# Performance work log

Measured on AMD Instinct MI355X. Metric: run time of the kernel, lower is better.

## Reference

```python
import jax, jax.numpy as jnp
import numpy as np
import math

B, L, C = 2, 4096, 256
H = 4            # n_head
K = 4            # Chebyshev kernel size
GROUPS = 32      # GroupNorm groups
EPS = 1e-5


def group_norm(x, gamma, beta):
    # x: [B, L, C]; stats per (batch, group) over (L, C//G), as torch GroupNorm
    # applied to x.permute(0, 2, 1) -> [B, C, L].
    b, l, c = x.shape
    xg = x.reshape(b, l, GROUPS, c // GROUPS)
    mean = xg.mean(axis=(1, 3), keepdims=True)
    var = xg.var(axis=(1, 3), keepdims=True)
    xg = (xg - mean) * jax.lax.rsqrt(var + EPS)
    return xg.reshape(b, l, c) * gamma + beta


def cheb_conv(lap, x, w):
    # Chebyshev graph conv: x [B, L, Fin], lap [L, L], w [K, Fin, Fout]
    xt = [x]
    if w.shape[0] > 1:
        xt.append(jnp.einsum('uv,bvc->buc', lap, x))
    for _ in range(2, w.shape[0]):
        xt.append(2.0 * jnp.einsum('uv,bvc->buc', lap, xt[-1]) - xt[-2])
    xs = jnp.stack(xt, axis=0)                       # [K, B, L, Fin]
    return jnp.einsum('kblc,kcf->blf', xs, w)        # [B, L, Fout]


def setup_inputs() -> dict:
    key = jax.random.key(0)
    ks = jax.random.split(key, 4)
    x = jax.random.normal(ks[0], (B, L, C), dtype=jnp.float32)
    # symmetric, spectrally well-behaved stand-in Laplacian
    a = jax.random.normal(ks[1], (L, L), dtype=jnp.float32) / jnp.sqrt(jnp.float32(L))
    lap = 0.5 * (a + a.T)
    gamma = jnp.ones((C,), dtype=jnp.float32)
    beta = jnp.zeros((C,), dtype=jnp.float32)
    w_qkv = jax.random.normal(ks[2], (K, C, 3 * C), dtype=jnp.float32) * (1.0 / math.sqrt(C * K))
    w_out = jax.random.normal(ks[3], (K, C, C), dtype=jnp.float32) * (1.0 / math.sqrt(C * K))
    return {"x": x, "lap": lap, "gamma": gamma, "beta": beta,
            "w_qkv": w_qkv, "w_out": w_out}


def reference(x, lap, gamma, beta, w_qkv, w_out):
    b, l, c = x.shape
    hd = c // H
    norm = group_norm(x, gamma, beta)
    qkv = cheb_conv(lap, norm, w_qkv).reshape(b, l, H, 3 * hd)
    q, k, v = jnp.split(qkv, 3, axis=3)              # each [B, L, H, hd]
    attn = jnp.einsum('blnc,bmnc->blmn', q, k) / math.sqrt(c)  # [B, L, M, H]
    # faithful to torch: view(B, L, H, -1) re-splits contiguous (M, H) as (H, M)
    attn = jax.nn.softmax(attn.reshape(b, l, H, -1), axis=-1)
    attn = attn.reshape(b, l, l, H)
    out = jnp.einsum('blmn,bmnc->blnc', attn, v).reshape(b, l, c)
    out = cheb_conv(lap, out, w_out)
    return out + x
```

## Files before the change

### kernel.cpp

```cpp
#include <hip/hip_runtime.h>
#include <hip/hip_bf16.h>
#include <stdint.h>

#define L 4096
#define C 256
#define NH 4
#define F3 768
#define KC 1024

typedef __attribute__((ext_vector_type(4))) float f32x4;
typedef __attribute__((ext_vector_type(8))) short short8;
typedef unsigned short u16;

__device__ __forceinline__ u16 f2bf(float f) {
  union { float f; unsigned u; } v; v.f = f;
  unsigned r = v.u + 0x7FFFu + ((v.u >> 16) & 1u);
  return (u16)(r >> 16);
}
__device__ __forceinline__ float bf2f(u16 b) {
  union { unsigned u; float f; } v; v.u = ((unsigned)b) << 16;
  return v.f;
}
__device__ __forceinline__ u16 f2bf_rne(float f) {
  __hip_bfloat16 h = __float2bfloat16(f);
  return *(u16*)&h;
}

__device__ __forceinline__ void glds16(const u16* g, u16* lds_base_uniform) {
  __builtin_amdgcn_global_load_lds(
      (const __attribute__((address_space(1))) void*)g,
      (__attribute__((address_space(3))) void*)lds_base_uniform, 16, 0, 0);
}


__global__ __launch_bounds__(256) void tobf16_kernel(const float* __restrict__ src, u16* __restrict__ dst, long n) {
  long i = ((long)blockIdx.x * 256 + threadIdx.x) * 8;
  if (i >= n) return;
  float4 a = *(const float4*)(src + i);
  float4 c = *(const float4*)(src + i + 4);
  u16 o[8] = {f2bf(a.x),f2bf(a.y),f2bf(a.z),f2bf(a.w),f2bf(c.x),f2bf(c.y),f2bf(c.z),f2bf(c.w)};
  *(int4*)(dst + i) = *(int4*)o;
}

__global__ __launch_bounds__(256) void transpose_w_kernel(const float* __restrict__ src, u16* __restrict__ dst, int F) {
  int idx = blockIdx.x * 256 + threadIdx.x;
  if (idx >= F * KC) return;
  int f = idx / KC, kc = idx - f * KC;
  dst[idx] = f2bf(src[(long)kc * F + f]);
}

__global__ __launch_bounds__(256) void gn_stats(const float* __restrict__ x, float* __restrict__ st) {
  const int b = blockIdx.x >> 5, g = blockIdx.x & 31, ch = blockIdx.y;
  const int tid = threadIdx.x;
  const float* xb = x + (long)b * L * C + g * 8;
  float s = 0.f, sq = 0.f;
  for (int l = ch * 512 + tid; l < ch * 512 + 512; l += 256) {
    const float4* p = (const float4*)(xb + (long)l * C);
    float4 a = p[0], c = p[1];
    s  += a.x + a.y + a.z + a.w + c.x + c.y + c.z + c.w;
    sq += a.x*a.x + a.y*a.y + a.z*a.z + a.w*a.w + c.x*c.x + c.y*c.y + c.z*c.z + c.w*c.w;
  }
  __shared__ float rs[256], rq[256];
  rs[tid] = s; rq[tid] = sq;
  __syncthreads();
  for (int o = 128; o > 0; o >>= 1) {
    if (tid < o) { rs[tid] += rs[tid + o]; rq[tid] += rq[tid + o]; }
    __syncthreads();
  }
  if (tid == 0) {
    st[(blockIdx.x * 8 + ch) * 2 + 0] = rs[0];
    st[(blockIdx.x * 8 + ch) * 2 + 1] = rq[0];
  }
}

__global__ __launch_bounds__(256) void gn_apply(const float* __restrict__ x, const float* __restrict__ gamma,
                                                const float* __restrict__ beta, const float* __restrict__ st,
                                                u16* __restrict__ normT, u16* __restrict__ xt_nt) {
  const int b = blockIdx.x >> 5, g = blockIdx.x & 31, ch = blockIdx.y;
  const int tid = threadIdx.x;
  float s = 0.f, sq = 0.f;
#pragma unroll
  for (int j = 0; j < 8; ++j) {
    s  += st[(blockIdx.x * 8 + j) * 2 + 0];
    sq += st[(blockIdx.x * 8 + j) * 2 + 1];
  }
  const float mean = s * (1.f / 32768.f);
  const float var  = sq * (1.f / 32768.f) - mean * mean;
  const float rsig = rsqrtf(var + 1e-5f);
  float gm[8], bt[8];
#pragma unroll
  for (int j = 0; j < 8; ++j) { gm[j] = gamma[g*8+j] * rsig; bt[j] = beta[g*8+j]; }
  const float* xb = x + (long)b * L * C + g * 8;
  for (int l = ch * 512 + tid; l < ch * 512 + 512; l += 256) {
    const float4* p = (const float4*)(xb + (long)l * C);
    float4 a = p[0], c = p[1];
    float v[8] = {a.x,a.y,a.z,a.w,c.x,c.y,c.z,c.w};
    u16 o8[8];
#pragma unroll
    for (int j = 0; j < 8; ++j) o8[j] = f2bf((v[j] - mean) * gm[j] + bt[j]);
    *(int4*)(xt_nt + ((long)b * L + l) * KC + g * 8) = *(int4*)o8;
#pragma unroll
    for (int j = 0; j < 8; ++j) normT[(long)(b * C + g * 8 + j) * L + l] = o8[j];
  }
}

#define BM 128
#define BN 128
#define BK 64

template<int OUT_BF16, int QSCALE, int SPLITK>
__global__ __launch_bounds__(256) void gemm_bt(const u16* __restrict__ A, const u16* __restrict__ BT,
                                               void* __restrict__ Cv, int M, int N, int Kc, int Ktot) {
  __shared__ u16 Al[BM * BK];
  __shared__ u16 Bl[BN * BK];
  const int tid = threadIdx.x;
  const int lane = tid & 63;
  const int wid = tid >> 6;
  const int wr = (wid >> 1) * 64;
  const int wc = (wid & 1) * 64;
  const long bm = (long)blockIdx.x * BM;
  const long bn = (long)blockIdx.y * BN;
  const int k_beg = SPLITK ? blockIdx.z * Kc : 0;
  const int k_end = k_beg + Kc;
  const int jrow = lane & 15, jk = lane >> 4;
  const int lr8 = lane >> 3, lsl = lane & 7;
  f32x4 acc[4][4] = {};

  for (int k0 = k_beg; k0 < k_end; k0 += BK) {
#pragma unroll
    for (int j = 0; j < 4; ++j) {
      int chunk = wid * 4 + j;
      int r = chunk * 8 + lr8;
      glds16(A + (bm + r) * (long)Ktot + k0 + ((lsl ^ (r & 7)) * 8), Al + chunk * 512);
    }
#pragma unroll
    for (int j = 0; j < 4; ++j) {
      int chunk = wid * 4 + j;
      int r = chunk * 8 + lr8;
      glds16(BT + (bn + r) * (long)Ktot + k0 + ((lsl ^ (r & 7)) * 8), Bl + chunk * 512);
    }
    __syncthreads();
    short8 af[4][2], bfr[4][2];
#pragma unroll
    for (int rt = 0; rt < 4; ++rt)
#pragma unroll
      for (int kc = 0; kc < 2; ++kc) {
        int r = wr + rt * 16 + jrow;
        int sl = kc * 4 + jk;
        af[rt][kc] = *(short8*)(Al + r * 64 + ((sl ^ (r & 7)) * 8));
      }
#pragma unroll
    for (int ct = 0; ct < 4; ++ct)
#pragma unroll
      for (int kc = 0; kc < 2; ++kc) {
        int r = wc + ct * 16 + jrow;
        int sl = kc * 4 + jk;
        bfr[ct][kc] = *(short8*)(Bl + r * 64 + ((sl ^ (r & 7)) * 8));
      }
#pragma unroll
    for (int kc = 0; kc < 2; ++kc)
#pragma unroll
      for (int rt = 0; rt < 4; ++rt)
#pragma unroll
        for (int ct = 0; ct < 4; ++ct)
          acc[rt][ct] = __builtin_amdgcn_mfma_f32_16x16x32_bf16(af[rt][kc], bfr[ct][kc], acc[rt][ct], 0, 0, 0);
    __syncthreads();
  }
  float* outf = SPLITK ? ((float*)Cv + (long)blockIdx.z * M * N) : (float*)Cv;
#pragma unroll
  for (int rt = 0; rt < 4; ++rt)
#pragma unroll
    for (int ct = 0; ct < 4; ++ct)
#pragma unroll
      for (int r = 0; r < 4; ++r) {
        long row = bm + wr + rt * 16 + 4 * jk + r;
        long col = bn + wc + ct * 16 + jrow;
        float v = acc[rt][ct][r];
        if (QSCALE) { if ((int)(col % 192) < 64) v *= 0.0625f; }
        if (OUT_BF16) ((u16*)Cv)[row * N + col] = f2bf(v);
        else outf[row * N + col] = v;
      }
}

__global__ __launch_bounds__(256) void cheb_combine(const float* __restrict__ Yp, const u16* __restrict__ prevT,
                                                    u16* __restrict__ outT, u16* __restrict__ xt_nt,
                                                    int kslot, float coef) {
  __shared__ u16 t[64][65];
  const int r0 = blockIdx.x * 64, c0 = blockIdx.y * 64;
  const int tid = threadIdx.x;
  const long pl = 512L * L;
#pragma unroll
  for (int s = 0; s < 16; ++s) {
    int idx = s * 256 + tid;
    int r = idx >> 6, c = idx & 63;
    long off = (long)(r0 + r) * L + c0 + c;
    float v = coef * (Yp[off] + Yp[pl + off] + Yp[2 * pl + off] + Yp[3 * pl + off]);
    if (prevT) v -= bf2f(prevT[off]);
    u16 u = f2bf(v);
    outT[off] = u;
    t[r][c] = u;
  }
  __syncthreads();
  const int b = r0 >> 8, ch0 = r0 & 255;
#pragma unroll
  for (int s = 0; s < 16; ++s) {
    int idx = s * 256 + tid;
    int lr = idx >> 6, cc = idx & 63;
    xt_nt[((long)b * L + c0 + lr) * KC + kslot * C + ch0 + cc] = t[cc][lr];
  }
}

__global__ __launch_bounds__(256) void out_combine(const float* __restrict__ Yp, const float* __restrict__ x,
                                                   float* __restrict__ out) {
  const long pl = 2097152L;
  long i = ((long)blockIdx.x * 256 + threadIdx.x) * 4;
  float4 a = *(const float4*)(Yp + i);
  float4 b = *(const float4*)(Yp + pl + i);
  float4 c = *(const float4*)(Yp + 2 * pl + i);
  float4 d = *(const float4*)(Yp + 3 * pl + i);
  float4 xr = *(const float4*)(x + i);
  float4 o;
  o.x = a.x + b.x + c.x + d.x + xr.x;
  o.y = a.y + b.y + c.y + d.y + xr.y;
  o.z = a.z + b.z + c.z + d.z + xr.z;
  o.w = a.w + b.w + c.w + d.w + xr.w;
  *(float4*)(out + i) = o;
}

__global__ __launch_bounds__(256) void vt_kernel(const u16* __restrict__ qkv, u16* __restrict__ VT) {
  __shared__ u16 t[64][65];
  const int bh = blockIdx.x;
  const int b = bh >> 2, h = bh & 3;
  const int m0 = blockIdx.y * 64;
  const int tid = threadIdx.x;
#pragma unroll
  for (int s = 0; s < 16; ++s) {
    int idx = s * 256 + tid; int mr = idx >> 6, cc = idx & 63;
    t[mr][cc] = qkv[((long)b * L + m0 + mr) * F3 + h * 192 + 128 + cc];
  }
  __syncthreads();
#pragma unroll
  for (int s = 0; s < 16; ++s) {
    int idx = s * 256 + tid; int cr = idx >> 6, mm = idx & 63;
    VT[((long)bh * 64 + cr) * L + m0 + mm] = t[mm][cr];
  }
}

__global__ __launch_bounds__(256) void attn_kernel(const u16* __restrict__ qkv, const u16* __restrict__ VT,
                                                   u16* __restrict__ part) {
  const int b = blockIdx.z;
  const int g = blockIdx.y;
  const int l0 = blockIdx.x * 64;
  const int tid = threadIdx.x;
  const int lane = tid & 63;
  const int h = tid >> 6;
  const int jrow = lane & 15, jk = lane >> 4;

  __shared__ u16 P_lds[4][64][72];
  __shared__ float ssm[4][64];

  short8 aq[4][2];
#pragma unroll
  for (int rt = 0; rt < 4; ++rt)
#pragma unroll
    for (int kc = 0; kc < 2; ++kc)
      aq[rt][kc] = *(const short8*)(qkv + ((long)b * L + l0 + rt * 16 + jrow) * F3 + h * 192 + kc * 32 + jk * 8);

  const u16* Kbase = qkv + (long)b * L * F3 + h * 192 + 64;
  const u16* Vbase = VT + (long)(b * 4 + h) * 64 * L;

  f32x4 gac[4][4] = {};
  float psum[4] = {0.f, 0.f, 0.f, 0.f};

#pragma unroll 2
  for (int mc = 0; mc < 16; ++mc) {
    const int m0 = g * 1024 + mc * 64;
    short8 kf[4][2];
#pragma unroll
    for (int kt = 0; kt < 4; ++kt)
#pragma unroll
      for (int kc = 0; kc < 2; ++kc)
        kf[kt][kc] = *(const short8*)(Kbase + (long)(m0 + kt * 16 + jrow) * F3 + kc * 32 + jk * 8);
    short8 vf[4][2];
#pragma unroll
    for (int ct = 0; ct < 4; ++ct)
#pragma unroll
      for (int km = 0; km < 2; ++km)
        vf[ct][km] = *(const short8*)(Vbase + (long)(ct * 16 + jrow) * L + m0 + km * 32 + jk * 8);

#pragma unroll
    for (int rt = 0; rt < 4; ++rt) {
      f32x4 st[4] = {};
#pragma unroll
      for (int kc = 0; kc < 2; ++kc)
#pragma unroll
        for (int kt = 0; kt < 4; ++kt)
          st[kt] = __builtin_amdgcn_mfma_f32_16x16x32_bf16(kf[kt][kc], aq[rt][kc], st[kt], 0, 0, 0);
#pragma unroll
      for (int kt = 0; kt < 4; ++kt) {
        float p0 = __expf(st[kt][0]);
        float p1 = __expf(st[kt][1]);
        float p2 = __expf(st[kt][2]);
        float p3 = __expf(st[kt][3]);
        psum[rt] += (p0 + p1) + (p2 + p3);
        u16 pk[4] = {f2bf_rne(p0), f2bf_rne(p1), f2bf_rne(p2), f2bf_rne(p3)};
        *(uint2*)&P_lds[h][rt * 16 + jrow][kt * 16 + jk * 4] = *(uint2*)pk;
      }
    }
    short8 pa[4][2];
#pragma unroll
    for (int rt = 0; rt < 4; ++rt)
#pragma unroll
      for (int km = 0; km < 2; ++km)
        pa[rt][km] = *(short8*)&P_lds[h][rt * 16 + jrow][km * 32 + jk * 8];
#pragma unroll
    for (int km = 0; km < 2; ++km)
#pragma unroll
      for (int rt = 0; rt < 4; ++rt)
#pragma unroll
        for (int ct = 0; ct < 4; ++ct)
          gac[rt][ct] = __builtin_amdgcn_mfma_f32_16x16x32_bf16(pa[rt][km], vf[ct][km], gac[rt][ct], 0, 0, 0);
  }

#pragma unroll
  for (int rt = 0; rt < 4; ++rt) {
    float s = psum[rt];
    s += __shfl_xor(s, 16);
    s += __shfl_xor(s, 32);
    psum[rt] = s;
  }
  if (jk == 0) {
#pragma unroll
    for (int rt = 0; rt < 4; ++rt) ssm[h][rt * 16 + jrow] = psum[rt];
  }
  __syncthreads();
  float scl[4][4];
#pragma unroll
  for (int rt = 0; rt < 4; ++rt)
#pragma unroll
    for (int r = 0; r < 4; ++r) {
      int row = rt * 16 + jk * 4 + r;
      scl[rt][r] = 1.f / (ssm[0][row] + ssm[1][row] + ssm[2][row] + ssm[3][row]);
    }
#pragma unroll
  for (int rt = 0; rt < 4; ++rt)
#pragma unroll
    for (int ct = 0; ct < 4; ++ct) {
      u16 pk[4];
#pragma unroll
      for (int r = 0; r < 4; ++r) pk[r] = f2bf_rne(gac[rt][ct][r] * scl[rt][r]);
      *(uint2*)(part + (long)g * (512L * L)
                + (long)(b * C + h * 64 + ct * 16 + jrow) * L + l0 + rt * 16 + jk * 4) = *(uint2*)pk;
    }
}

__global__ __launch_bounds__(256) void attn_reduce(const u16* __restrict__ part, u16* __restrict__ attnT,
                                                   u16* __restrict__ xt_nt) {
  __shared__ u16 t[64][65];
  const int r0 = blockIdx.x * 64, c0 = blockIdx.y * 64;
  const int tid = threadIdx.x;
  const long gs = 512L * L;
#pragma unroll
  for (int s = 0; s < 16; ++s) {
    int idx = s * 256 + tid;
    int r = idx >> 6, c = idx & 63;
    long off = (long)(r0 + r) * L + c0 + c;
    float v = bf2f(part[off]) + bf2f(part[gs + off]) + bf2f(part[2 * gs + off]) + bf2f(part[3 * gs + off]);
    u16 u = f2bf(v);
    attnT[off] = u;
    t[r][c] = u;
  }
  __syncthreads();
  const int b = r0 >> 8, ch0 = r0 & 255;
#pragma unroll
  for (int s = 0; s < 16; ++s) {
    int idx = s * 256 + tid;
    int lr = idx >> 6, cc = idx & 63;
    xt_nt[((long)b * L + c0 + lr) * KC + 0 * C + ch0 + cc] = t[cc][lr];
  }
}


extern "C" void kernel_launch(void* const* d_in, const int* in_sizes, int n_in,
                              void* d_out, int out_size, void* d_ws, size_t ws_size,
                              hipStream_t stream) {
  const float* x     = (const float*)d_in[0];
  const float* lap   = (const float*)d_in[1];
  const float* gamma = (const float*)d_in[2];
  const float* beta  = (const float*)d_in[3];
  const float* w_qkv = (const float*)d_in[4];
  const float* w_out = (const float*)d_in[5];
  float* out = (float*)d_out;

  char* ws = (char*)d_ws;
  u16*   lap_bf = (u16*)ws;   ws += (size_t)L * L * 2;
  u16*   xt_nt  = (u16*)ws;   ws += (size_t)2 * L * KC * 2;
  u16*   xtT0   = (u16*)ws;   ws += (size_t)512 * L * 2;
  u16*   xtT1   = (u16*)ws;   ws += (size_t)512 * L * 2;
  u16*   xtT2   = (u16*)ws;   ws += (size_t)512 * L * 2;
  u16*   xtT3   = (u16*)ws;   ws += (size_t)512 * L * 2;
  char*  regA   = ws;         ws += (size_t)32 * 1024 * 1024;
  u16*   WqkvT  = (u16*)ws;   ws += (size_t)F3 * KC * 2;
  u16*   WoutT  = (u16*)ws;   ws += (size_t)C * KC * 2;
  float* gnst   = (float*)ws; ws += (size_t)64 * 8 * 2 * 4;

  float* Ypart  = (float*)regA;
  u16*   qkv_bf = (u16*)regA;
  u16*   VTb    = qkv_bf + (size_t)2 * L * F3;
  u16*   part   = (u16*)(regA + 16777216);

  tobf16_kernel<<<dim3(8192), dim3(256), 0, stream>>>(lap, lap_bf, (long)L * L);
  transpose_w_kernel<<<dim3((F3 * KC + 255) / 256), dim3(256), 0, stream>>>(w_qkv, WqkvT, F3);
  transpose_w_kernel<<<dim3((C * KC + 255) / 256), dim3(256), 0, stream>>>(w_out, WoutT, C);
  gn_stats<<<dim3(64, 8), dim3(256), 0, stream>>>(x, gnst);
  gn_apply<<<dim3(64, 8), dim3(256), 0, stream>>>(x, gamma, beta, gnst, xtT0, xt_nt);

  gemm_bt<0,0,1><<<dim3(4, 32, 4), dim3(256), 0, stream>>>(xtT0, lap_bf, Ypart, 512, L, 1024, L);
  cheb_combine<<<dim3(8, 64), dim3(256), 0, stream>>>(Ypart, nullptr, xtT1, xt_nt, 1, 1.f);
  gemm_bt<0,0,1><<<dim3(4, 32, 4), dim3(256), 0, stream>>>(xtT1, lap_bf, Ypart, 512, L, 1024, L);
  cheb_combine<<<dim3(8, 64), dim3(256), 0, stream>>>(Ypart, xtT0, xtT2, xt_nt, 2, 2.f);
  gemm_bt<0,0,1><<<dim3(4, 32, 4), dim3(256), 0, stream>>>(xtT2, lap_bf, Ypart, 512, L, 1024, L);
  cheb_combine<<<dim3(8, 64), dim3(256), 0, stream>>>(Ypart, xtT1, xtT3, xt_nt, 3, 2.f);

  gemm_bt<1,1,0><<<dim3(64, 6), dim3(256), 0, stream>>>(xt_nt, WqkvT, qkv_bf, 2 * L, F3, KC, KC);
  vt_kernel<<<dim3(8, 64), dim3(256), 0, stream>>>(qkv_bf, VTb);

  attn_kernel<<<dim3(64, 4, 2), dim3(256), 0, stream>>>(qkv_bf, VTb, part);
  attn_reduce<<<dim3(8, 64), dim3(256), 0, stream>>>(part, xtT0, xt_nt);

  gemm_bt<0,0,1><<<dim3(4, 32, 4), dim3(256), 0, stream>>>(xtT0, lap_bf, Ypart, 512, L, 1024, L);
  cheb_combine<<<dim3(8, 64), dim3(256), 0, stream>>>(Ypart, nullptr, xtT1, xt_nt, 1, 1.f);
  gemm_bt<0,0,1><<<dim3(4, 32, 4), dim3(256), 0, stream>>>(xtT1, lap_bf, Ypart, 512, L, 1024, L);
  cheb_combine<<<dim3(8, 64), dim3(256), 0, stream>>>(Ypart, xtT0, xtT2, xt_nt, 2, 2.f);
  gemm_bt<0,0,1><<<dim3(4, 32, 4), dim3(256), 0, stream>>>(xtT2, lap_bf, Ypart, 512, L, 1024, L);
  cheb_combine<<<dim3(8, 64), dim3(256), 0, stream>>>(Ypart, xtT1, xtT3, xt_nt, 3, 2.f);

  gemm_bt<0,0,1><<<dim3(64, 2, 4), dim3(256), 0, stream>>>(xt_nt, WoutT, Ypart, 2 * L, C, 256, KC);
  out_combine<<<dim3(2048), dim3(256), 0, stream>>>(Ypart, x, out);
}
```

Measured before the change: 410.5 us.

## Halve GEMM N-tile, use two-way split-K with bf16 partial sums

Shrinks the GEMM tile from 128x128 to 128x64 and changes the split-K factor from four to two, doubling the N-grid so the block count stays the same. Split-K partials are now stored as bf16 instead of fp32, and the combine kernels read only two bf16 planes. The aim is to cut the partial-sum write and read traffic and give each block a longer K loop. In exchange, partial sums are rounded to bf16 before the reduction, which costs accuracy, and the smaller tile reuses each loaded A tile across fewer columns.

```diff
diff --git a/kernel.cpp b/kernel.cpp
--- a/kernel.cpp
+++ b/kernel.cpp
@@ -105,7 +105,7 @@
 }
 
 #define BM 128
-#define BN 128
+#define BN 64
 #define BK 64
 
 template<int OUT_BF16, int QSCALE, int SPLITK>
@@ -117,14 +117,14 @@
   const int lane = tid & 63;
   const int wid = tid >> 6;
   const int wr = (wid >> 1) * 64;
-  const int wc = (wid & 1) * 64;
+  const int wc = (wid & 1) * 32;
   const long bm = (long)blockIdx.x * BM;
   const long bn = (long)blockIdx.y * BN;
   const int k_beg = SPLITK ? blockIdx.z * Kc : 0;
   const int k_end = k_beg + Kc;
   const int jrow = lane & 15, jk = lane >> 4;
   const int lr8 = lane >> 3, lsl = lane & 7;
-  f32x4 acc[4][4] = {};
+  f32x4 acc[4][2] = {};
 
   for (int k0 = k_beg; k0 < k_end; k0 += BK) {
 #pragma unroll
@@ -134,13 +134,13 @@
       glds16(A + (bm + r) * (long)Ktot + k0 + ((lsl ^ (r & 7)) * 8), Al + chunk * 512);
     }
 #pragma unroll
-    for (int j = 0; j < 4; ++j) {
-      int chunk = wid * 4 + j;
+    for (int j = 0; j < 2; ++j) {
+      int chunk = wid * 2 + j;
       int r = chunk * 8 + lr8;
       glds16(BT + (bn + r) * (long)Ktot + k0 + ((lsl ^ (r & 7)) * 8), Bl + chunk * 512);
     }
     __syncthreads();
-    short8 af[4][2], bfr[4][2];
+    short8 af[4][2], bfr[2][2];
 #pragma unroll
     for (int rt = 0; rt < 4; ++rt)
 #pragma unroll
@@ -150,7 +150,7 @@
         af[rt][kc] = *(short8*)(Al + r * 64 + ((sl ^ (r & 7)) * 8));
       }
 #pragma unroll
-    for (int ct = 0; ct < 4; ++ct)
+    for (int ct = 0; ct < 2; ++ct)
 #pragma unroll
       for (int kc = 0; kc < 2; ++kc) {
         int r = wc + ct * 16 + jrow;
@@ -162,27 +162,27 @@
 #pragma unroll
       for (int rt = 0; rt < 4; ++rt)
 #pragma unroll
-        for (int ct = 0; ct < 4; ++ct)
+        for (int ct = 0; ct < 2; ++ct)
           acc[rt][ct] = __builtin_amdgcn_mfma_f32_16x16x32_bf16(af[rt][kc], bfr[ct][kc], acc[rt][ct], 0, 0, 0);
     __syncthreads();
   }
-  float* outf = SPLITK ? ((float*)Cv + (long)blockIdx.z * M * N) : (float*)Cv;
 #pragma unroll
   for (int rt = 0; rt < 4; ++rt)
 #pragma unroll
-    for (int ct = 0; ct < 4; ++ct)
+    for (int ct = 0; ct < 2; ++ct)
 #pragma unroll
       for (int r = 0; r < 4; ++r) {
         long row = bm + wr + rt * 16 + 4 * jk + r;
         long col = bn + wc + ct * 16 + jrow;
         float v = acc[rt][ct][r];
         if (QSCALE) { if ((int)(col % 192) < 64) v *= 0.0625f; }
-        if (OUT_BF16) ((u16*)Cv)[row * N + col] = f2bf(v);
-        else outf[row * N + col] = v;
+        if (SPLITK) ((u16*)Cv)[(long)blockIdx.z * M * N + row * N + col] = f2bf(v);
+        else if (OUT_BF16) ((u16*)Cv)[row * N + col] = f2bf(v);
+        else ((float*)Cv)[row * N + col] = v;
       }
 }
 
-__global__ __launch_bounds__(256) void cheb_combine(const float* __restrict__ Yp, const u16* __restrict__ prevT,
+__global__ __launch_bounds__(256) void cheb_combine(const u16* __restrict__ Yp, const u16* __restrict__ prevT,
                                                     u16* __restrict__ outT, u16* __restrict__ xt_nt,
                                                     int kslot, float coef) {
   __shared__ u16 t[64][65];
@@ -194,7 +194,7 @@
     int idx = s * 256 + tid;
     int r = idx >> 6, c = idx & 63;
     long off = (long)(r0 + r) * L + c0 + c;
-    float v = coef * (Yp[off] + Yp[pl + off] + Yp[2 * pl + off] + Yp[3 * pl + off]);
+    float v = coef * (bf2f(Yp[off]) + bf2f(Yp[pl + off]));
     if (prevT) v -= bf2f(prevT[off]);
     u16 u = f2bf(v);
     outT[off] = u;
@@ -210,20 +210,20 @@
   }
 }
 
-__global__ __launch_bounds__(256) void out_combine(const float* __restrict__ Yp, const float* __restrict__ x,
+__global__ __launch_bounds__(256) void out_combine(const u16* __restrict__ Yp, const float* __restrict__ x,
                                                    float* __restrict__ out) {
   const long pl = 2097152L;
   long i = ((long)blockIdx.x * 256 + threadIdx.x) * 4;
-  float4 a = *(const float4*)(Yp + i);
-  float4 b = *(const float4*)(Yp + pl + i);
-  float4 c = *(const float4*)(Yp + 2 * pl + i);
-  float4 d = *(const float4*)(Yp + 3 * pl + i);
+  uint2 w0 = *(const uint2*)(Yp + i);
+  uint2 w1 = *(const uint2*)(Yp + pl + i);
+  const u16* a = (const u16*)&w0;
+  const u16* b = (const u16*)&w1;
   float4 xr = *(const float4*)(x + i);
   float4 o;
-  o.x = a.x + b.x + c.x + d.x + xr.x;
-  o.y = a.y + b.y + c.y + d.y + xr.y;
-  o.z = a.z + b.z + c.z + d.z + xr.z;
-  o.w = a.w + b.w + c.w + d.w + xr.w;
+  o.x = bf2f(a[0]) + bf2f(b[0]) + xr.x;
+  o.y = bf2f(a[1]) + bf2f(b[1]) + xr.y;
+  o.z = bf2f(a[2]) + bf2f(b[2]) + xr.z;
+  o.w = bf2f(a[3]) + bf2f(b[3]) + xr.w;
   *(float4*)(out + i) = o;
 }
 
@@ -404,7 +404,7 @@
   u16*   WoutT  = (u16*)ws;   ws += (size_t)C * KC * 2;
   float* gnst   = (float*)ws; ws += (size_t)64 * 8 * 2 * 4;
 
-  float* Ypart  = (float*)regA;
+  u16*   Ypart  = (u16*)regA;
   u16*   qkv_bf = (u16*)regA;
   u16*   VTb    = qkv_bf + (size_t)2 * L * F3;
   u16*   part   = (u16*)(regA + 16777216);
@@ -415,26 +415,26 @@
   gn_stats<<<dim3(64, 8), dim3(256), 0, stream>>>(x, gnst);
   gn_apply<<<dim3(64, 8), dim3(256), 0, stream>>>(x, gamma, beta, gnst, xtT0, xt_nt);
 
-  gemm_bt<0,0,1><<<dim3(4, 32, 4), dim3(256), 0, stream>>>(xtT0, lap_bf, Ypart, 512, L, 1024, L);
+  gemm_bt<0,0,1><<<dim3(4, 64, 2), dim3(256), 0, stream>>>(xtT0, lap_bf, Ypart, 512, L, 2048, L);
   cheb_combine<<<dim3(8, 64), dim3(256), 0, stream>>>(Ypart, nullptr, xtT1, xt_nt, 1, 1.f);
-  gemm_bt<0,0,1><<<dim3(4, 32, 4), dim3(256), 0, stream>>>(xtT1, lap_bf, Ypart, 512, L, 1024, L);
+  gemm_bt<0,0,1><<<dim3(4, 64, 2), dim3(256), 0, stream>>>(xtT1, lap_bf, Ypart, 512, L, 2048, L);
   cheb_combine<<<dim3(8, 64), dim3(256), 0, stream>>>(Ypart, xtT0, xtT2, xt_nt, 2, 2.f);
-  gemm_bt<0,0,1><<<dim3(4, 32, 4), dim3(256), 0, stream>>>(xtT2, lap_bf, Ypart, 512, L, 1024, L);
+  gemm_bt<0,0,1><<<dim3(4, 64, 2), dim3(256), 0, stream>>>(xtT2, lap_bf, Ypart, 512, L, 2048, L);
   cheb_combine<<<dim3(8, 64), dim3(256), 0, stream>>>(Ypart, xtT1, xtT3, xt_nt, 3, 2.f);
 
-  gemm_bt<1,1,0><<<dim3(64, 6), dim3(256), 0, stream>>>(xt_nt, WqkvT, qkv_bf, 2 * L, F3, KC, KC);
+  gemm_bt<1,1,0><<<dim3(64, 12), dim3(256), 0, stream>>>(xt_nt, WqkvT, qkv_bf, 2 * L, F3, KC, KC);
   vt_kernel<<<dim3(8, 64), dim3(256), 0, stream>>>(qkv_bf, VTb);
 
   attn_kernel<<<dim3(64, 4, 2), dim3(256), 0, stream>>>(qkv_bf, VTb, part);
   attn_reduce<<<dim3(8, 64), dim3(256), 0, stream>>>(part, xtT0, xt_nt);
 
-  gemm_bt<0,0,1><<<dim3(4, 32, 4), dim3(256), 0, stream>>>(xtT0, lap_bf, Ypart, 512, L, 1024, L);
+  gemm_bt<0,0,1><<<dim3(4, 64, 2), dim3(256), 0, stream>>>(xtT0, lap_bf, Ypart, 512, L, 2048, L);
   cheb_combine<<<dim3(8, 64), dim3(256), 0, stream>>>(Ypart, nullptr, xtT1, xt_nt, 1, 1.f);
-  gemm_bt<0,0,1><<<dim3(4, 32, 4), dim3(256), 0, stream>>>(xtT1, lap_bf, Ypart, 512, L, 1024, L);
+  gemm_bt<0,0,1><<<dim3(4, 64, 2), dim3(256), 0, stream>>>(xtT1, lap_bf, Ypart, 512, L, 2048, L);
   cheb_combine<<<dim3(8, 64), dim3(256), 0, stream>>>(Ypart, xtT0, xtT2, xt_nt, 2, 2.f);
-  gemm_bt<0,0,1><<<dim3(4, 32, 4), dim3(256), 0, stream>>>(xtT2, lap_bf, Ypart, 512, L, 1024, L);
+  gemm_bt<0,0,1><<<dim3(4, 64, 2), dim3(256), 0, stream>>>(xtT2, lap_bf, Ypart, 512, L, 2048, L);
   cheb_combine<<<dim3(8, 64), dim3(256), 0, stream>>>(Ypart, xtT1, xtT3, xt_nt, 3, 2.f);
 
-  gemm_bt<0,0,1><<<dim3(64, 2, 4), dim3(256), 0, stream>>>(xt_nt, WoutT, Ypart, 2 * L, C, 256, KC);
+  gemm_bt<0,0,1><<<dim3(64, 4, 2), dim3(256), 0, stream>>>(xt_nt, WoutT, Ypart, 2 * L, C, 512, KC);
   out_combine<<<dim3(2048), dim3(256), 0, stream>>>(Ypart, x, out);
 }
```

New measurement: 423.7 us. 3.2% more time.
